# Optimization experiments

Hardware: AMD Instinct MI355X
Metric: run time of the kernel (lower is better)

Reference implementation:

```python
import jax, jax.numpy as jnp
import numpy as np

SEQ, B, H = 2048, 2, 4096
N_HEADS = 32
N_KV = 2
HEAD_DIM = H // N_HEADS          # 128
ROT_DIM = HEAD_DIM // 2          # 64 (rope cache last-2 dim = 32 pairs)


def setup_inputs() -> dict:
    key = jax.random.key(0)
    ks = jax.random.split(key, 8)
    hidden_states = jax.random.normal(ks[0], (SEQ, B, H), dtype=jnp.float32)
    rotary_pos_emb = jax.random.normal(ks[1], (SEQ, 1, ROT_DIM // 2, 2), dtype=jnp.float32)
    s = 0.02
    Wq = jax.random.normal(ks[2], (H, H), dtype=jnp.float32) * s
    bq = jnp.zeros((H,), dtype=jnp.float32)
    Wk = jax.random.normal(ks[3], (H, N_KV * HEAD_DIM), dtype=jnp.float32) * s
    bk = jnp.zeros((N_KV * HEAD_DIM,), dtype=jnp.float32)
    Wv = jax.random.normal(ks[4], (H, N_KV * HEAD_DIM), dtype=jnp.float32) * s
    bv = jnp.zeros((N_KV * HEAD_DIM,), dtype=jnp.float32)
    Wo = jax.random.normal(ks[5], (H, H), dtype=jnp.float32) * s
    return {"hidden_states": hidden_states, "rotary_pos_emb": rotary_pos_emb,
            "Wq": Wq, "bq": bq, "Wk": Wk, "bk": bk, "Wv": Wv, "bv": bv, "Wo": Wo}


def _apply_rope(x, rope):
    # x: [sq, b, np, hn]; rope: [sq, 1, rot/2, 2]
    sq = x.shape[0]
    rot = rope.shape[-2] * 2
    x_rot, x_pass = x[..., :rot], x[..., rot:]
    xs = x_rot.reshape(x.shape[0], x.shape[1], x.shape[2], rot // 2, 2)
    rc = rope[:sq].reshape(sq, -1, 1, rot // 2, 2)  # [sq,1,1,rot/2,2]
    o0 = xs[..., 0] * rc[..., 0] - xs[..., 1] * rc[..., 1]
    o1 = xs[..., 1] * rc[..., 0] + xs[..., 0] * rc[..., 1]
    out = jnp.stack([o0, o1], axis=-1).reshape(x_rot.shape)
    return jnp.concatenate([out, x_pass], axis=-1)


def reference(hidden_states, rotary_pos_emb, Wq, bq, Wk, bk, Wv, bv, Wo):
    sq, b, h = hidden_states.shape
    group = N_HEADS // N_KV

    q = (hidden_states @ Wq + bq).reshape(sq, b, N_HEADS, HEAD_DIM)
    k = (hidden_states @ Wk + bk).reshape(sq, b, N_KV, HEAD_DIM)
    v = (hidden_states @ Wv + bv).reshape(sq, b, N_KV, HEAD_DIM)

    q = _apply_rope(q, rotary_pos_emb)
    k = _apply_rope(k, rotary_pos_emb)

    # GQA expand: head index = kv_head * group + g (matches expand+view in torch)
    k = jnp.repeat(k, group, axis=2)  # [sq, b, N_HEADS, hd]
    v = jnp.repeat(v, group, axis=2)

    scale = 1.0 / np.sqrt(HEAD_DIM)
    scores = jnp.einsum("sbhd,tbhd->bhst", q, k) * scale  # [b, nh, sq, sq]
    causal = jnp.tril(jnp.ones((sq, sq), dtype=bool))
    scores = jnp.where(causal, scores, jnp.finfo(scores.dtype).min)
    probs = jax.nn.softmax(scores, axis=-1)
    ctx = jnp.einsum("bhst,tbhd->sbhd", probs, v)  # [sq, b, nh, hd]
    ctx = ctx.reshape(sq, b, h)
    return ctx @ Wo
```

## Files before the change

### kernel.cpp

```cpp
#include <hip/hip_runtime.h>
#include <stdint.h>

#define SEQ   2048
#define BATCH 2
#define HD    4096
#define NH    32
#define NKV   2
#define HDIM  128
#define NT    (SEQ*BATCH)
#define KVC   (NKV*HDIM)

typedef short  bf16x8 __attribute__((ext_vector_type(8)));
typedef short  sh4    __attribute__((ext_vector_type(4)));
typedef float  f32x4  __attribute__((ext_vector_type(4)));
typedef float  f32x16 __attribute__((ext_vector_type(16)));

__device__ __forceinline__ float bf2f(unsigned short u){
  union { unsigned int i; float f; } v; v.i = ((unsigned int)u) << 16; return v.f;
}
__device__ __forceinline__ unsigned short f2bf(float f){
  union { float f; unsigned int i; } v; v.f = f;
  unsigned int r = v.i + 0x7FFFu + ((v.i >> 16) & 1u);
  return (unsigned short)(r >> 16);
}
__device__ __forceinline__ unsigned int cvtpk_bf16(float lo, float hi){
  unsigned int r;
  asm("v_cvt_pk_bf16_f32 %0, %1, %2" : "=v"(r) : "v"(lo), "v"(hi));
  return r;
}
__device__ __forceinline__ void plane_swap(unsigned int &a, unsigned int &b){
  asm("v_permlane32_swap_b32 %0, %1" : "+v"(a), "+v"(b));
}
__device__ __forceinline__ bf16x8 mk_pf(float a0f,float a1f,float a2f,float a3f,
                                        float b0f,float b1f,float b2f,float b3f){
  unsigned int a0 = cvtpk_bf16(a0f, a1f);
  unsigned int a1 = cvtpk_bf16(a2f, a3f);
  unsigned int b0 = cvtpk_bf16(b0f, b1f);
  unsigned int b1 = cvtpk_bf16(b2f, b3f);
  plane_swap(a0, b0);
  plane_swap(a1, b1);
  union { unsigned int u[4]; bf16x8 h; } u;
  u.u[0] = a0; u.u[1] = a1; u.u[2] = b0; u.u[3] = b1;
  return u.h;
}

__device__ __forceinline__ void gload_lds16(const void* g, void* lds){
  __builtin_amdgcn_global_load_lds(
      (const __attribute__((address_space(1))) unsigned int*)(size_t)g,
      (__attribute__((address_space(3))) unsigned int*)(unsigned int)(size_t)lds,
      16, 0, 0);
}

__device__ __forceinline__ void BARRIER(){
  __builtin_amdgcn_sched_barrier(0);
  asm volatile("" ::: "memory");
  __builtin_amdgcn_s_barrier();
  asm volatile("" ::: "memory");
  __builtin_amdgcn_sched_barrier(0);
}
#define VMCNT(N) do { asm volatile("s_waitcnt vmcnt(" #N ")" ::: "memory"); \
                      __builtin_amdgcn_sched_barrier(0); } while(0)

__global__ void k_cast(const float* __restrict__ in, unsigned short* __restrict__ out, int n4){
  int i = blockIdx.x * blockDim.x + threadIdx.x;
  if (i >= n4) return;
  float4 v = ((const float4*)in)[i];
  ushort4 o; o.x = f2bf(v.x); o.y = f2bf(v.y); o.z = f2bf(v.z); o.w = f2bf(v.w);
  ((ushort4*)out)[i] = o;
}

__global__ void k_transpose(const float* __restrict__ W, unsigned short* __restrict__ WT,
                            int K, int N){
  __shared__ float t[32][33];
  int n0 = blockIdx.x * 32, k0 = blockIdx.y * 32;
  int tx = threadIdx.x, ty = threadIdx.y;
  t[ty][tx] = W[(size_t)(k0 + ty) * N + n0 + tx];
  __syncthreads();
  WT[(size_t)(n0 + ty) * K + k0 + tx] = f2bf(t[tx][ty]);
}

template<bool OUTF32>
__global__ __launch_bounds__(256) void k_gemm(
    const unsigned short* __restrict__ A,
    const unsigned short* __restrict__ BT,
    const float* __restrict__ bias,
    const float* __restrict__ bias2, int bsplit,
    void* __restrict__ C, int M, int N, int K)
{
  __shared__ unsigned short As[128*32];
  __shared__ unsigned short Bs[128*32];
  const int tid  = threadIdx.x;
  const int lane = tid & 63;
  const int w    = tid >> 6;
  const int l4   = lane >> 4, l15 = lane & 15;
  const int wm   = (w >> 1) * 64, wn = (w & 1) * 64;
  const size_t bm = (size_t)blockIdx.y * 128, bn = (size_t)blockIdx.x * 128;

  f32x4 acc[4][4] = {};
  const int scol = (lane & 3) * 8;

  for (int k0 = 0; k0 < K; k0 += 32) {
    #pragma unroll
    for (int j = 0; j < 2; ++j) {
      const int r = w*32 + j*16 + (lane >> 2);
      gload_lds16(A  + (bm + r) * (size_t)K + k0 + scol, As + (size_t)(w*32 + j*16) * 32);
      gload_lds16(BT + (bn + r) * (size_t)K + k0 + scol, Bs + (size_t)(w*32 + j*16) * 32);
    }
    __syncthreads();
    bf16x8 af[4], bfr[4];
    #pragma unroll
    for (int m = 0; m < 4; ++m)
      af[m] = *(const bf16x8*)(As + (wm + m*16 + l15)*32 + l4*8);
    #pragma unroll
    for (int n = 0; n < 4; ++n)
      bfr[n] = *(const bf16x8*)(Bs + (wn + n*16 + l15)*32 + l4*8);
    #pragma unroll
    for (int m = 0; m < 4; ++m)
      #pragma unroll
      for (int n = 0; n < 4; ++n)
        acc[m][n] = __builtin_amdgcn_mfma_f32_16x16x32_bf16(af[m], bfr[n], acc[m][n], 0, 0, 0);
    __syncthreads();
  }

  #pragma unroll
  for (int n = 0; n < 4; ++n) {
    const size_t col = bn + wn + n*16 + l15;
    float badd = 0.0f;
    if (bias) badd = (bias2 && (int)col >= bsplit) ? bias2[col - bsplit] : bias[col];
    #pragma unroll
    for (int m = 0; m < 4; ++m) {
      const size_t row0 = bm + wm + m*16 + l4*4;
      #pragma unroll
      for (int r = 0; r < 4; ++r) {
        float v = acc[m][n][r] + badd;
        if (OUTF32) ((float*)C)[(row0 + r) * (size_t)N + col] = v;
        else ((unsigned short*)C)[(row0 + r) * (size_t)N + col] = f2bf(v);
      }
    }
  }
}

template<bool OUTF32>
__global__ __launch_bounds__(512, 2) void k_gemm256(
    const unsigned short* __restrict__ A,
    const unsigned short* __restrict__ BT,
    const float* __restrict__ bias,
    void* __restrict__ C, int M, int N, int K)
{
  __shared__ __attribute__((aligned(16))) unsigned short As[2][16384];
  __shared__ __attribute__((aligned(16))) unsigned short Bs[2][16384];
  const int tid  = threadIdx.x;
  const int lane = tid & 63;
  const int w    = tid >> 6;
  const int c    = lane & 15, g = lane >> 4;
  const int wm   = w >> 2, wn = w & 3;

  const int nwg = (int)(gridDim.x * gridDim.y);
  int bid = (int)(blockIdx.y * gridDim.x + blockIdx.x);
  if ((nwg & 7) == 0) bid = (bid & 7) * (nwg >> 3) + (bid >> 3);
  const int bx = bid % (int)gridDim.x, by = bid / (int)gridDim.x;
  const size_t bm = (size_t)by * 256, bn = (size_t)bx * 256;

  const char* Ab = (const char*)(A  + bm * (size_t)K);
  const char* Bb = (const char*)(BT + bn * (size_t)K);
  const size_t Kb2 = (size_t)K * 2;
  const int cswz = (c & 7) << 4;

  f32x4 acc[8][4] = {};
  bf16x8 af[4][2], bfr[4][2];

#define STAGE_A(bi, h, k0) do { \
    _Pragma("unroll") \
    for (int _j = 0; _j < 2; ++_j) { \
      const int _i = _j*512 + tid; \
      const int _row = (h)*128 + (_i >> 3); \
      const int _ch  = _i & 7; \
      gload_lds16(Ab + (size_t)_row * Kb2 + (size_t)(k0)*2 + ((_ch*16) ^ ((_row & 7) << 4)), \
                  (char*)As[bi] + (h)*16384 + _j*8192 + w*1024); \
    } } while(0)
#define STAGE_B(bi, h, k0) do { \
    _Pragma("unroll") \
    for (int _j = 0; _j < 2; ++_j) { \
      const int _i = _j*512 + tid; \
      const int _row = (h)*128 + (_i >> 3); \
      const int _ch  = _i & 7; \
      gload_lds16(Bb + (size_t)_row * Kb2 + (size_t)(k0)*2 + ((_ch*16) ^ ((_row & 7) << 4)), \
                  (char*)Bs[bi] + (h)*16384 + _j*8192 + w*1024); \
    } } while(0)
#define LDA(bi, mg) do { \
    _Pragma("unroll") \
    for (int _m = 0; _m < 4; ++_m) { \
      const char* _p = (const char*)As[bi] + (size_t)(((mg)*128 + _m*32 + wm*16 + c) * 128); \
      af[_m][0] = *(const bf16x8*)(_p + (( 0 + g*16) ^ cswz)); \
      af[_m][1] = *(const bf16x8*)(_p + ((64 + g*16) ^ cswz)); \
    } } while(0)
#define LDB(bi, ng) do { \
    _Pragma("unroll") \
    for (int _n = 0; _n < 2; ++_n) { \
      const char* _p = (const char*)Bs[bi] + (size_t)((((ng)*2+_n)*64 + wn*16 + c) * 128); \
      bfr[(ng)*2+_n][0] = *(const bf16x8*)(_p + (( 0 + g*16) ^ cswz)); \
      bfr[(ng)*2+_n][1] = *(const bf16x8*)(_p + ((64 + g*16) ^ cswz)); \
    } } while(0)
#define MFMA16(mg, ng) do { \
    __builtin_amdgcn_s_setprio(1); \
    _Pragma("unroll") \
    for (int _m = 0; _m < 4; ++_m) \
      _Pragma("unroll") \
      for (int _n = 0; _n < 2; ++_n) { \
        acc[(mg)*4+_m][(ng)*2+_n] = __builtin_amdgcn_mfma_f32_16x16x32_bf16( \
            af[_m][0], bfr[(ng)*2+_n][0], acc[(mg)*4+_m][(ng)*2+_n], 0, 0, 0); \
        acc[(mg)*4+_m][(ng)*2+_n] = __builtin_amdgcn_mfma_f32_16x16x32_bf16( \
            af[_m][1], bfr[(ng)*2+_n][1], acc[(mg)*4+_m][(ng)*2+_n], 0, 0, 0); \
      } \
    __builtin_amdgcn_s_setprio(0); \
  } while(0)

  STAGE_A(0, 0, 0);
  STAGE_B(0, 0, 0);
  STAGE_B(0, 1, 0);
  STAGE_A(0, 1, 0);
  STAGE_A(1, 0, 64);
  STAGE_B(1, 0, 64);
  VMCNT(8);
  BARRIER();

  const int niter = K >> 7;
  for (int it = 0; it < niter; ++it) {
    const int kb = it*128 + 64;
    int k2 = it*128 + 128; if (k2 >= K) k2 = 0;
    int k3 = it*128 + 192; if (k3 >= K) k3 = 0;
    LDA(0, 0); LDB(0, 0);
    STAGE_A(1, 1, kb);
    BARRIER();
    MFMA16(0, 0);
    VMCNT(6);
    BARRIER();
    LDB(0, 1);
    STAGE_B(1, 1, kb);
    BARRIER();
    MFMA16(0, 1);
    BARRIER();
    LDA(0, 1);
    STAGE_A(0, 0, k2);
    BARRIER();
    MFMA16(1, 0);
    BARRIER();
    STAGE_B(0, 0, k2);
    BARRIER();
    MFMA16(1, 1);
    VMCNT(8);
    BARRIER();
    LDA(1, 0); LDB(1, 0);
    STAGE_A(0, 1, k2);
    BARRIER();
    MFMA16(0, 0);
    VMCNT(6);
    BARRIER();
    LDB(1, 1);
    STAGE_B(0, 1, k2);
    BARRIER();
    MFMA16(0, 1);
    BARRIER();
    LDA(1, 1);
    STAGE_A(1, 0, k3);
    BARRIER();
    MFMA16(1, 0);
    BARRIER();
    STAGE_B(1, 0, k3);
    BARRIER();
    MFMA16(1, 1);
    VMCNT(8);
    BARRIER();
  }

  #pragma unroll
  for (int m = 0; m < 8; ++m) {
    const size_t row0 = bm + m*32 + wm*16 + g*4;
    #pragma unroll
    for (int n = 0; n < 4; ++n) {
      const size_t col = bn + n*64 + wn*16 + c;
      const float badd = bias ? bias[col] : 0.0f;
      #pragma unroll
      for (int r = 0; r < 4; ++r) {
        float v = acc[m][n][r] + badd;
        if (OUTF32) ((float*)C)[(row0 + r) * (size_t)N + col] = v;
        else ((unsigned short*)C)[(row0 + r) * (size_t)N + col] = f2bf(v);
      }
    }
  }
#undef STAGE_A
#undef STAGE_B
#undef LDA
#undef LDB
#undef MFMA16
}

__global__ void k_rope(const unsigned short* __restrict__ In, const float* __restrict__ rope,
                       unsigned short* __restrict__ Out, int ldin, int ncols, int nslab,
                       int psh, float sc)
{
  int idx = blockIdx.x * 256 + threadIdx.x;
  int npair = ncols >> 1;
  if (idx >= NT * npair) return;
  int t = idx >> psh, pr = idx & (npair - 1);
  int colp = pr * 2, h = colp >> 7, d = colp & 127;
  int s = t >> 1, b = t & 1;
  float x0 = bf2f(In[(size_t)t * ldin + colp]);
  float x1 = bf2f(In[(size_t)t * ldin + colp + 1]);
  float o0 = x0, o1 = x1;
  if (d < 64) {
    int i2 = d >> 1;
    float cr = rope[((size_t)s * 32 + i2) * 2 + 0];
    float ci = rope[((size_t)s * 32 + i2) * 2 + 1];
    o0 = x0 * cr - x1 * ci;
    o1 = x1 * cr + x0 * ci;
  }
  size_t dst = ((size_t)(b * nslab + h) * SEQ + s) * HDIM + d;
  Out[dst]     = f2bf(o0 * sc);
  Out[dst + 1] = f2bf(o1 * sc);
}

__global__ void k_vt(const unsigned short* __restrict__ In, int ld,
                     unsigned short* __restrict__ Out){
  int idx = blockIdx.x * 256 + threadIdx.x;
  if (idx >= NT * KVC) return;
  int t = idx >> 8, cp = idx & 255;
  int kv = cp >> 7, d = cp & 127;
  int s = t >> 1, b = t & 1;
  Out[((size_t)(b * NKV + kv) * HDIM + d) * SEQ + s] = In[(size_t)t * ld + cp];
}

__global__ __launch_bounds__(256, 2) void k_attn(
    const unsigned short* __restrict__ Q,
    const unsigned short* __restrict__ Kk,
    const unsigned short* __restrict__ Vt,
    unsigned short* __restrict__ Ctx)
{
  const int tid  = threadIdx.x;
  const int lane = tid & 63;
  const int w    = tid >> 6;
  const int l31  = lane & 31;
  const int hi   = lane >> 5;
  const int bh = blockIdx.y;
  const int b = bh >> 5, h = bh & 31;
  const int qb  = (int)(gridDim.x - 1 - blockIdx.x);
  const int qw0 = qb * 128 + w * 32;

  const unsigned short* Qb = Q  + ((size_t)(b * NH  + h)        * SEQ + qw0) * HDIM;
  const char* Kb = (const char*)(Kk + ((size_t)(b * NKV + (h >> 4)) * SEQ) * HDIM);
  const char* Vb = (const char*)(Vt + ((size_t)(b * NKV + (h >> 4)) * HDIM) * SEQ);

  __shared__ unsigned short Ks[64*128];
  __shared__ unsigned short Vs[128*64];

  bf16x8 qf[8];
  #pragma unroll
  for (int kk = 0; kk < 8; ++kk)
    qf[kk] = *(const bf16x8*)(Qb + (size_t)l31 * HDIM + kk*16 + hi*8);

  f32x16 of0 = {}, of1 = {}, of2 = {}, of3 = {};
  float mrun = -1e30f, lrun = 0.0f;
  const int qmax = qw0 + 31;
  const int qg   = qw0 + l31;
  const int tblk = qb * 128 + 128;

  const int kr = lane >> 4, kc = lane & 15;
  const int vr = lane >> 3, vc = lane & 7;
  const int rswz = (l31 & 7) << 4;

  for (int t0 = 0; t0 < tblk; t0 += 64) {
    #pragma unroll
    for (int j = 0; j < 4; ++j) {
      const int r = w*16 + j*4 + kr;
      gload_lds16(Kb + (size_t)(t0 + r) * 256 + ((kc*16) ^ ((r & 7) << 4)),
                  (char*)Ks + (w*16 + j*4) * 256);
    }
    #pragma unroll
    for (int j = 0; j < 4; ++j) {
      const int d = w*32 + j*8 + vr;
      gload_lds16(Vb + (size_t)d * (SEQ*2) + (size_t)t0*2 + ((vc*16) ^ ((d & 7) << 4)),
                  (char*)Vs + (w*32 + j*8) * 128);
    }
    __syncthreads();

    if (t0 <= qmax) {
      f32x16 s0 = {};
      #pragma unroll
      for (int kk = 0; kk < 8; ++kk) {
        bf16x8 kf = *(const bf16x8*)((const char*)Ks + l31*256 + ((kk*32 + hi*16) ^ rswz));
        s0 = __builtin_amdgcn_mfma_f32_32x32x16_bf16(kf, qf[kk], s0, 0, 0, 0);
      }
      const int qh0 = qg - t0 - 4*hi;
      if (t0 + 31 > qw0) {
        #pragma unroll
        for (int r = 0; r < 16; ++r) {
          const int tc = (r & 3) + 8*(r >> 2);
          if (tc > qh0) s0[r] = -1e30f;
        }
      }
      const bool act1 = (t0 + 32 <= qmax);
      f32x16 s1 = {};
      if (act1) {
        #pragma unroll
        for (int kk = 0; kk < 8; ++kk) {
          bf16x8 kf = *(const bf16x8*)((const char*)Ks + (32 + l31)*256 + ((kk*32 + hi*16) ^ rswz));
          s1 = __builtin_amdgcn_mfma_f32_32x32x16_bf16(kf, qf[kk], s1, 0, 0, 0);
        }
        if (t0 + 63 > qw0) {
          const int qh1 = qh0 - 32;
          #pragma unroll
          for (int r = 0; r < 16; ++r) {
            const int tc = (r & 3) + 8*(r >> 2);
            if (tc > qh1) s1[r] = -1e30f;
          }
        }
      }
      float mloc = s0[0];
      #pragma unroll
      for (int r = 1; r < 16; ++r) mloc = fmaxf(mloc, s0[r]);
      if (act1) {
        #pragma unroll
        for (int r = 0; r < 16; ++r) mloc = fmaxf(mloc, s1[r]);
      }
      mloc = fmaxf(mloc, __shfl_xor(mloc, 32));
      if (!__all(mloc - mrun <= 8.0f)) {
        const float mn = fmaxf(mrun, mloc);
        const float al = exp2f(mrun - mn);
        mrun = mn;
        lrun *= al;
        of0 *= al; of1 *= al; of2 *= al; of3 *= al;
      }
      float ps = 0.0f;
      float p0[16];
      #pragma unroll
      for (int r = 0; r < 16; ++r) { p0[r] = exp2f(s0[r] - mrun); ps += p0[r]; }
      const bf16x8 pf0 = mk_pf(p0[0],p0[1],p0[2],p0[3],   p0[4],p0[5],p0[6],p0[7]);
      const bf16x8 pf1 = mk_pf(p0[8],p0[9],p0[10],p0[11], p0[12],p0[13],p0[14],p0[15]);
      bf16x8 pf2, pf3;
      if (act1) {
        float p1[16];
        #pragma unroll
        for (int r = 0; r < 16; ++r) { p1[r] = exp2f(s1[r] - mrun); ps += p1[r]; }
        pf2 = mk_pf(p1[0],p1[1],p1[2],p1[3],   p1[4],p1[5],p1[6],p1[7]);
        pf3 = mk_pf(p1[8],p1[9],p1[10],p1[11], p1[12],p1[13],p1[14],p1[15]);
      }
      ps += __shfl_xor(ps, 32);
      lrun += ps;

#define PVDT(ofv, dt) do { \
        const char* _vrow = (const char*)Vs + (size_t)(((dt)*32 + l31) * 128); \
        bf16x8 _v0 = *(const bf16x8*)(_vrow + (( 0 + hi*16) ^ rswz)); \
        bf16x8 _v1 = *(const bf16x8*)(_vrow + ((32 + hi*16) ^ rswz)); \
        ofv = __builtin_amdgcn_mfma_f32_32x32x16_bf16(_v0, pf0, ofv, 0, 0, 0); \
        ofv = __builtin_amdgcn_mfma_f32_32x32x16_bf16(_v1, pf1, ofv, 0, 0, 0); \
        if (act1) { \
          bf16x8 _v2 = *(const bf16x8*)(_vrow + ((64 + hi*16) ^ rswz)); \
          bf16x8 _v3 = *(const bf16x8*)(_vrow + ((96 + hi*16) ^ rswz)); \
          ofv = __builtin_amdgcn_mfma_f32_32x32x16_bf16(_v2, pf2, ofv, 0, 0, 0); \
          ofv = __builtin_amdgcn_mfma_f32_32x32x16_bf16(_v3, pf3, ofv, 0, 0, 0); \
        } } while(0)
      PVDT(of0, 0);
      PVDT(of1, 1);
      PVDT(of2, 2);
      PVDT(of3, 3);
#undef PVDT
    }
    __syncthreads();
  }

  const float inv = 1.0f / lrun;
  unsigned short* Crow = Ctx + ((size_t)(qg * BATCH + b)) * HD + (size_t)h * HDIM;
#define EPI(ofv, dt) do { \
    _Pragma("unroll") \
    for (int _q = 0; _q < 4; ++_q) { \
      const int _col = (dt)*32 + 8*_q + 4*hi; \
      const unsigned int _w0 = cvtpk_bf16(ofv[4*_q+0]*inv, ofv[4*_q+1]*inv); \
      const unsigned int _w1 = cvtpk_bf16(ofv[4*_q+2]*inv, ofv[4*_q+3]*inv); \
      *(unsigned int*)(Crow + _col)     = _w0; \
      *(unsigned int*)(Crow + _col + 2) = _w1; \
    } } while(0)
  EPI(of0, 0);
  EPI(of1, 1);
  EPI(of2, 2);
  EPI(of3, 3);
#undef EPI
}

extern "C" void kernel_launch(void* const* d_in, const int* in_sizes, int n_in,
                              void* d_out, int out_size, void* d_ws, size_t ws_size,
                              hipStream_t stream)
{
  const float* hs   = (const float*)d_in[0];
  const float* rope = (const float*)d_in[1];
  const float* Wq   = (const float*)d_in[2];
  const float* bq   = (const float*)d_in[3];
  const float* Wk   = (const float*)d_in[4];
  const float* bk   = (const float*)d_in[5];
  const float* Wv   = (const float*)d_in[6];
  const float* bv   = (const float*)d_in[7];
  const float* Wo   = (const float*)d_in[8];

  char* ws = (char*)d_ws;
  const size_t MB = (size_t)1 << 20;
  unsigned short* Xbf  = (unsigned short*)(ws);
  unsigned short* Ctx  = Xbf;
  unsigned short* WqT  = (unsigned short*)(ws + 32*MB);
  unsigned short* Qa   = WqT;
  unsigned short* WkT  = (unsigned short*)(ws + 64*MB);
  unsigned short* WvT  = (unsigned short*)(ws + 66*MB);
  unsigned short* WoT  = (unsigned short*)(ws + 68*MB);
  unsigned short* Qtmp = (unsigned short*)(ws + 100*MB);
  unsigned short* KVt  = (unsigned short*)(ws + 132*MB);
  unsigned short* Ka   = (unsigned short*)(ws + 136*MB);
  unsigned short* VTa  = (unsigned short*)(ws + 138*MB);

  k_cast<<<(NT*HD/4 + 255)/256, 256, 0, stream>>>(hs, Xbf, NT*HD/4);

  dim3 tb(32, 32);
  k_transpose<<<dim3(HD/32,  HD/32), tb, 0, stream>>>(Wq, WqT, HD, HD);
  k_transpose<<<dim3(KVC/32, HD/32), tb, 0, stream>>>(Wk, WkT, HD, KVC);
  k_transpose<<<dim3(KVC/32, HD/32), tb, 0, stream>>>(Wv, WvT, HD, KVC);
  k_transpose<<<dim3(HD/32,  HD/32), tb, 0, stream>>>(Wo, WoT, HD, HD);

  k_gemm256<false><<<dim3(HD/256, NT/256), 512, 0, stream>>>(Xbf, WqT, bq, Qtmp, NT, HD, HD);
  k_gemm<false><<<dim3(512/128, NT/128), 256, 0, stream>>>(Xbf, WkT, bk, bv, 256,
                                                           KVt, NT, 512, HD);

  const float scq = 0.08838834764831845f * 1.4426950408889634f;
  k_rope<<<(NT*(HD/2)  + 255)/256, 256, 0, stream>>>(Qtmp, rope, Qa, HD, HD, NH, 11, scq);
  k_rope<<<(NT*(KVC/2) + 255)/256, 256, 0, stream>>>(KVt, rope, Ka, 512, KVC, NKV, 7, 1.0f);
  k_vt  <<<(NT*KVC     + 255)/256, 256, 0, stream>>>(KVt + 256, 512, VTa);

  k_attn<<<dim3(SEQ/128, NH*BATCH), 256, 0, stream>>>(Qa, Ka, VTa, Ctx);

  k_gemm256<true><<<dim3(HD/256, NT/256), 512, 0, stream>>>(Ctx, WoT, nullptr, d_out, NT, HD, HD);
}
```

Before: 604.3 us.

## Fuse Q/K/V projections into one GEMM and rebalance attention block order

Drops the separate 128-tile K/V GEMM and runs Q, K and V through the pipelined 256-tile GEMM over a concatenated 4608-wide transposed weight. This works because WqT, WkT and WvT sit contiguously in the workspace. The epilogue picks the right bias and splits output columns into the Q buffer and the KV buffer. Attention now interleaves heavy and light causal query blocks across the grid to balance load, and the K tile in LDS uses a 16-row XOR swizzle to cut bank conflicts. The fused grid of 288 workgroups can leave a partial second wave on the device.

```diff
diff --git a/kernel.cpp b/kernel.cpp
--- a/kernel.cpp
+++ b/kernel.cpp
@@ -79,73 +79,15 @@
   WT[(size_t)(n0 + ty) * K + k0 + tx] = f2bf(t[tx][ty]);
 }
 
-template<bool OUTF32>
-__global__ __launch_bounds__(256) void k_gemm(
-    const unsigned short* __restrict__ A,
-    const unsigned short* __restrict__ BT,
-    const float* __restrict__ bias,
-    const float* __restrict__ bias2, int bsplit,
-    void* __restrict__ C, int M, int N, int K)
-{
-  __shared__ unsigned short As[128*32];
-  __shared__ unsigned short Bs[128*32];
-  const int tid  = threadIdx.x;
-  const int lane = tid & 63;
-  const int w    = tid >> 6;
-  const int l4   = lane >> 4, l15 = lane & 15;
-  const int wm   = (w >> 1) * 64, wn = (w & 1) * 64;
-  const size_t bm = (size_t)blockIdx.y * 128, bn = (size_t)blockIdx.x * 128;
-
-  f32x4 acc[4][4] = {};
-  const int scol = (lane & 3) * 8;
-
-  for (int k0 = 0; k0 < K; k0 += 32) {
-    #pragma unroll
-    for (int j = 0; j < 2; ++j) {
-      const int r = w*32 + j*16 + (lane >> 2);
-      gload_lds16(A  + (bm + r) * (size_t)K + k0 + scol, As + (size_t)(w*32 + j*16) * 32);
-      gload_lds16(BT + (bn + r) * (size_t)K + k0 + scol, Bs + (size_t)(w*32 + j*16) * 32);
-    }
-    __syncthreads();
-    bf16x8 af[4], bfr[4];
-    #pragma unroll
-    for (int m = 0; m < 4; ++m)
-      af[m] = *(const bf16x8*)(As + (wm + m*16 + l15)*32 + l4*8);
-    #pragma unroll
-    for (int n = 0; n < 4; ++n)
-      bfr[n] = *(const bf16x8*)(Bs + (wn + n*16 + l15)*32 + l4*8);
-    #pragma unroll
-    for (int m = 0; m < 4; ++m)
-      #pragma unroll
-      for (int n = 0; n < 4; ++n)
-        acc[m][n] = __builtin_amdgcn_mfma_f32_16x16x32_bf16(af[m], bfr[n], acc[m][n], 0, 0, 0);
-    __syncthreads();
-  }
-
-  #pragma unroll
-  for (int n = 0; n < 4; ++n) {
-    const size_t col = bn + wn + n*16 + l15;
-    float badd = 0.0f;
-    if (bias) badd = (bias2 && (int)col >= bsplit) ? bias2[col - bsplit] : bias[col];
-    #pragma unroll
-    for (int m = 0; m < 4; ++m) {
-      const size_t row0 = bm + wm + m*16 + l4*4;
-      #pragma unroll
-      for (int r = 0; r < 4; ++r) {
-        float v = acc[m][n][r] + badd;
-        if (OUTF32) ((float*)C)[(row0 + r) * (size_t)N + col] = v;
-        else ((unsigned short*)C)[(row0 + r) * (size_t)N + col] = f2bf(v);
-      }
-    }
-  }
-}
-
-template<bool OUTF32>
+template<int MODE>
 __global__ __launch_bounds__(512, 2) void k_gemm256(
     const unsigned short* __restrict__ A,
     const unsigned short* __restrict__ BT,
     const float* __restrict__ bias,
-    void* __restrict__ C, int M, int N, int K)
+    const float* __restrict__ bias2,
+    const float* __restrict__ bias3,
+    void* __restrict__ C, void* __restrict__ C2,
+    int M, int N, int K)
 {
   __shared__ __attribute__((aligned(16))) unsigned short As[2][16384];
   __shared__ __attribute__((aligned(16))) unsigned short Bs[2][16384];
@@ -278,13 +220,27 @@
     const size_t row0 = bm + m*32 + wm*16 + g*4;
     #pragma unroll
     for (int n = 0; n < 4; ++n) {
-      const size_t col = bn + n*64 + wn*16 + c;
-      const float badd = bias ? bias[col] : 0.0f;
+      const int col = (int)bn + n*64 + wn*16 + c;
+      float badd = 0.0f;
+      if (MODE == 2) {
+        badd = (col < 4096) ? bias[col]
+             : (col < 4352) ? bias2[col - 4096] : bias3[col - 4352];
+      } else if (bias) {
+        badd = bias[col];
+      }
       #pragma unroll
       for (int r = 0; r < 4; ++r) {
         float v = acc[m][n][r] + badd;
-        if (OUTF32) ((float*)C)[(row0 + r) * (size_t)N + col] = v;
-        else ((unsigned short*)C)[(row0 + r) * (size_t)N + col] = f2bf(v);
+        if (MODE == 1) {
+          ((float*)C)[(row0 + r) * (size_t)N + col] = v;
+        } else if (MODE == 0) {
+          ((unsigned short*)C)[(row0 + r) * (size_t)N + col] = f2bf(v);
+        } else {
+          if (col < 4096)
+            ((unsigned short*)C)[(row0 + r) * (size_t)4096 + col] = f2bf(v);
+          else
+            ((unsigned short*)C2)[(row0 + r) * (size_t)512 + (col - 4096)] = f2bf(v);
+        }
       }
     }
   }
@@ -343,7 +299,8 @@
   const int hi   = lane >> 5;
   const int bh = blockIdx.y;
   const int b = bh >> 5, h = bh & 31;
-  const int qb  = (int)(gridDim.x - 1 - blockIdx.x);
+  const int x = (int)blockIdx.x;
+  const int qb = (x & 1) ? (x >> 1) : ((int)gridDim.x - 1 - (x >> 1));
   const int qw0 = qb * 128 + w * 32;
 
   const unsigned short* Qb = Q  + ((size_t)(b * NH  + h)        * SEQ + qw0) * HDIM;
@@ -366,13 +323,14 @@
 
   const int kr = lane >> 4, kc = lane & 15;
   const int vr = lane >> 3, vc = lane & 7;
-  const int rswz = (l31 & 7) << 4;
+  const int rswzK = (l31 & 15) << 4;
+  const int rswzV = (l31 & 7) << 4;
 
   for (int t0 = 0; t0 < tblk; t0 += 64) {
     #pragma unroll
     for (int j = 0; j < 4; ++j) {
       const int r = w*16 + j*4 + kr;
-      gload_lds16(Kb + (size_t)(t0 + r) * 256 + ((kc*16) ^ ((r & 7) << 4)),
+      gload_lds16(Kb + (size_t)(t0 + r) * 256 + ((kc*16) ^ ((r & 15) << 4)),
                   (char*)Ks + (w*16 + j*4) * 256);
     }
     #pragma unroll
@@ -387,7 +345,7 @@
       f32x16 s0 = {};
       #pragma unroll
       for (int kk = 0; kk < 8; ++kk) {
-        bf16x8 kf = *(const bf16x8*)((const char*)Ks + l31*256 + ((kk*32 + hi*16) ^ rswz));
+        bf16x8 kf = *(const bf16x8*)((const char*)Ks + l31*256 + ((kk*32 + hi*16) ^ rswzK));
         s0 = __builtin_amdgcn_mfma_f32_32x32x16_bf16(kf, qf[kk], s0, 0, 0, 0);
       }
       const int qh0 = qg - t0 - 4*hi;
@@ -403,7 +361,7 @@
       if (act1) {
         #pragma unroll
         for (int kk = 0; kk < 8; ++kk) {
-          bf16x8 kf = *(const bf16x8*)((const char*)Ks + (32 + l31)*256 + ((kk*32 + hi*16) ^ rswz));
+          bf16x8 kf = *(const bf16x8*)((const char*)Ks + (32 + l31)*256 + ((kk*32 + hi*16) ^ rswzK));
           s1 = __builtin_amdgcn_mfma_f32_32x32x16_bf16(kf, qf[kk], s1, 0, 0, 0);
         }
         if (t0 + 63 > qw0) {
@@ -449,13 +407,13 @@
 
 #define PVDT(ofv, dt) do { \
         const char* _vrow = (const char*)Vs + (size_t)(((dt)*32 + l31) * 128); \
-        bf16x8 _v0 = *(const bf16x8*)(_vrow + (( 0 + hi*16) ^ rswz)); \
-        bf16x8 _v1 = *(const bf16x8*)(_vrow + ((32 + hi*16) ^ rswz)); \
+        bf16x8 _v0 = *(const bf16x8*)(_vrow + (( 0 + hi*16) ^ rswzV)); \
+        bf16x8 _v1 = *(const bf16x8*)(_vrow + ((32 + hi*16) ^ rswzV)); \
         ofv = __builtin_amdgcn_mfma_f32_32x32x16_bf16(_v0, pf0, ofv, 0, 0, 0); \
         ofv = __builtin_amdgcn_mfma_f32_32x32x16_bf16(_v1, pf1, ofv, 0, 0, 0); \
         if (act1) { \
-          bf16x8 _v2 = *(const bf16x8*)(_vrow + ((64 + hi*16) ^ rswz)); \
-          bf16x8 _v3 = *(const bf16x8*)(_vrow + ((96 + hi*16) ^ rswz)); \
+          bf16x8 _v2 = *(const bf16x8*)(_vrow + ((64 + hi*16) ^ rswzV)); \
+          bf16x8 _v3 = *(const bf16x8*)(_vrow + ((96 + hi*16) ^ rswzV)); \
           ofv = __builtin_amdgcn_mfma_f32_32x32x16_bf16(_v2, pf2, ofv, 0, 0, 0); \
           ofv = __builtin_amdgcn_mfma_f32_32x32x16_bf16(_v3, pf3, ofv, 0, 0, 0); \
         } } while(0)
@@ -505,9 +463,9 @@
   unsigned short* Xbf  = (unsigned short*)(ws);
   unsigned short* Ctx  = Xbf;
   unsigned short* WqT  = (unsigned short*)(ws + 32*MB);
-  unsigned short* Qa   = WqT;
   unsigned short* WkT  = (unsigned short*)(ws + 64*MB);
   unsigned short* WvT  = (unsigned short*)(ws + 66*MB);
+  unsigned short* Qa   = WqT;
   unsigned short* WoT  = (unsigned short*)(ws + 68*MB);
   unsigned short* Qtmp = (unsigned short*)(ws + 100*MB);
   unsigned short* KVt  = (unsigned short*)(ws + 132*MB);
@@ -522,9 +480,8 @@
   k_transpose<<<dim3(KVC/32, HD/32), tb, 0, stream>>>(Wv, WvT, HD, KVC);
   k_transpose<<<dim3(HD/32,  HD/32), tb, 0, stream>>>(Wo, WoT, HD, HD);
 
-  k_gemm256<false><<<dim3(HD/256, NT/256), 512, 0, stream>>>(Xbf, WqT, bq, Qtmp, NT, HD, HD);
-  k_gemm<false><<<dim3(512/128, NT/128), 256, 0, stream>>>(Xbf, WkT, bk, bv, 256,
-                                                           KVt, NT, 512, HD);
+  k_gemm256<2><<<dim3(4608/256, NT/256), 512, 0, stream>>>(
+      Xbf, WqT, bq, bk, bv, Qtmp, KVt, NT, 4608, HD);
 
   const float scq = 0.08838834764831845f * 1.4426950408889634f;
   k_rope<<<(NT*(HD/2)  + 255)/256, 256, 0, stream>>>(Qtmp, rope, Qa, HD, HD, NH, 11, scq);
@@ -533,5 +490,6 @@
 
   k_attn<<<dim3(SEQ/128, NH*BATCH), 256, 0, stream>>>(Qa, Ka, VTa, Ctx);
 
-  k_gemm256<true><<<dim3(HD/256, NT/256), 512, 0, stream>>>(Ctx, WoT, nullptr, d_out, NT, HD, HD);
-}
+  k_gemm256<1><<<dim3(HD/256, NT/256), 512, 0, stream>>>(
+      Ctx, WoT, nullptr, nullptr, nullptr, d_out, nullptr, NT, HD, HD);
+}
```

Measured after the change: 613.4 us. No clear change (+1.5%).
